# Optimization experiments

Hardware: AMD Instinct MI355X
Metric: run time of the kernel (lower is better)

Reference implementation:

```python
import jax, jax.numpy as jnp
import numpy as np

B, Q, H, W, C = 2, 8192, 64, 64, 64
C9 = C * 9
EPS = 1e-6


def _mlp(x, params):
    # gelu MLP, no activation on last layer (matches repo mlp)
    for Wm, b in params[:-1]:
        x = jax.nn.gelu(x @ Wm + b)
    Wl, bl = params[-1]
    return x @ Wl + bl


def _make_coord(h, w):
    # pixel-center coords in (-1,1); channel 0 = row dim, channel 1 = col dim
    hs = -1.0 + (2.0 * jnp.arange(h, dtype=jnp.float32) + 1.0) / h
    ws = -1.0 + (2.0 * jnp.arange(w, dtype=jnp.float32) + 1.0) / w
    return jnp.stack(jnp.meshgrid(hs, ws, indexing='ij'), axis=0)  # (2,h,w)


def _nearest_gather(feat, coord):
    # F.grid_sample(mode='nearest', align_corners=False) on a (B,1,q,2) grid.
    # feat (B,C,H,W); coord (B,q,2) with [...,0] indexing H, [...,1] indexing W
    h, w = feat.shape[-2], feat.shape[-1]
    ih = jnp.clip(jnp.round((coord[..., 0] + 1.0) * h / 2.0 - 0.5), 0, h - 1).astype(jnp.int32)
    iw = jnp.clip(jnp.round((coord[..., 1] + 1.0) * w / 2.0 - 0.5), 0, w - 1).astype(jnp.int32)
    return jax.vmap(lambda f, a, b: f[:, a, b].T)(feat, ih, iw)  # (B,q,C)


def _unfold3(feat):
    # F.unfold(feat, 3, padding=1).view(B, C*9, H, W): channel-major, kernel row-major
    b, c, h, w = feat.shape
    p = jnp.pad(feat, ((0, 0), (0, 0), (1, 1), (1, 1)))
    patches = jnp.stack([p[:, :, i:i + h, j:j + w] for i in range(3) for j in range(3)], axis=2)
    return patches.reshape(b, c * 9, h, w)


def _forward(inp, coord, scale, enc_w, enc_b, iw0, ib0, iw1, ib1, iw2, ib2,
             sw0, sb0, sw1, sb1, ww0, wb0, ww1, wb1):
    # encoder (stand-in conv3x3, 3 -> C feature channels)
    feat = jax.lax.conv_general_dilated(inp, enc_w, (1, 1), 'SAME',
                                        dimension_numbers=('NCHW', 'OIHW', 'NCHW'))
    feat = feat + enc_b[None, :, None, None]
    feat = _unfold3(feat)  # (B, C*9, H, W)
    bsz, cf, h, w = feat.shape
    fcoord = jnp.broadcast_to(_make_coord(h, w)[None], (bsz, 2, h, w))
    dims = jnp.array([h, w], dtype=feat.dtype)

    tx = (h - 1) / (1.0 - scale[:, 0, 0])  # (B,)
    ty = (w - 1) / (1.0 - scale[:, 0, 1])
    rx, ry = 1.0 / tx, 1.0 / ty
    scale_tok = scale * dims  # (B,q,2)

    imnet_p = [(iw0, ib0), (iw1, ib1), (iw2, ib2)]
    score_p = [(sw0, sb0), (sw1, sb1)]
    weight_p = [(ww0, wb0), (ww1, wb1)]

    preds = []
    for vx in (-1, 1):
        for vy in (-1, 1):
            shift = jnp.stack([vx * rx + EPS, vy * ry + EPS], axis=-1)[:, None, :]  # (B,1,2)
            c = jnp.clip(coord + shift, -1.0 + 1e-6, 1.0 - 1e-6)
            value = _nearest_gather(feat, c)      # (B,q,C*9)
            coord_k = _nearest_gather(fcoord, c)  # (B,q,2)
            rel = (coord - coord_k) * dims        # (B,q,2)
            score = _mlp(rel, score_p)            # (B,q,1) -> broadcast over 3
            mlp_in = jnp.concatenate([rel, scale_tok], axis=-1)  # (B,q,4)
            wmat = _mlp(mlp_in, imnet_p).reshape(bsz, -1, cf, 3)  # (B,q,C*9,3)
            preds.append(jnp.einsum('bqc,bqck->bqk', value, wmat) + score)
    stacked = jnp.stack(preds, axis=-1)  # (B,q,3,4)
    return _mlp(stacked, weight_p)[..., 0]  # (B,q,3)


def setup_inputs() -> dict:
    key = jax.random.key(0)
    ks = jax.random.split(key, 16)
    f32 = jnp.float32

    def wi(k, shape, fan_in):
        return jax.random.normal(k, shape, f32) / np.float32(np.sqrt(fan_in))

    return {
        'inp': jax.random.normal(ks[0], (B, 3, H, W), f32),
        'coord': jax.random.uniform(ks[1], (B, Q, 2), f32, -1.0 + 1e-4, 1.0 - 1e-4),
        'scale': jax.random.uniform(ks[2], (B, Q, 2), f32, 0.01, 0.05),
        'enc_w': wi(ks[3], (C, 3, 3, 3), 27),
        'enc_b': jnp.zeros((C,), f32),
        'iw0': wi(ks[4], (4, 256), 4), 'ib0': jnp.zeros((256,), f32),
        'iw1': wi(ks[5], (256, 256), 256), 'ib1': jnp.zeros((256,), f32),
        'iw2': wi(ks[6], (256, C9 * 3), 256), 'ib2': jnp.zeros((C9 * 3,), f32),
        'sw0': wi(ks[7], (2, 256), 2), 'sb0': jnp.zeros((256,), f32),
        'sw1': wi(ks[8], (256, 1), 256), 'sb1': jnp.zeros((1,), f32),
        'ww0': wi(ks[9], (4, 256), 4), 'wb0': jnp.zeros((256,), f32),
        'ww1': wi(ks[10], (256, 1), 256), 'wb1': jnp.zeros((1,), f32),
    }


def reference(inp, coord, scale, enc_w, enc_b, iw0, ib0, iw1, ib1, iw2, ib2,
              sw0, sb0, sw1, sb1, ww0, wb0, ww1, wb1):
    return _forward(inp, coord, scale, enc_w, enc_b, iw0, ib0, iw1, ib1, iw2, ib2,
                    sw0, sb0, sw1, sb1, ww0, wb0, ww1, wb1)
```

## Files before the change

kernel.cpp:

```cpp
#include <hip/hip_runtime.h>

#define QN 8192
#define CCH 64
#define NROW 65536
#define MR 64
#define NBLK (NROW / MR)
#define H0S 264
#define UW 784
#define SVP 592

typedef _Float16 f16x8 __attribute__((ext_vector_type(8)));
typedef _Float16 f16x4 __attribute__((ext_vector_type(4)));
typedef float f32x4 __attribute__((ext_vector_type(4)));

__device__ __forceinline__ float gelu_f(float x) {
    float x2 = x * x;
    float tt = fmaf(0.044715f, x2, 1.0f);
    float e = __builtin_amdgcn_exp2f(2.3022081597f * x * tt);
    float r = __builtin_amdgcn_rcpf(1.0f + e);
    return x - x * r;
}

__global__ __launch_bounds__(256) void k_pre(const float* __restrict__ inp,
                                             const float* __restrict__ ew,
                                             const float* __restrict__ eb,
                                             const float* __restrict__ coord,
                                             const float* __restrict__ scale,
                                             const float* __restrict__ sw0,
                                             const float* __restrict__ sb0,
                                             const float* __restrict__ sw1,
                                             const float* __restrict__ sb1,
                                             const float* __restrict__ iw1,
                                             const float* __restrict__ iw2,
                                             const float* __restrict__ ib2,
                                             float* __restrict__ featpad,
                                             float4* __restrict__ mlp_in,
                                             int2* __restrict__ ihiw,
                                             float* __restrict__ scoreg,
                                             _Float16* __restrict__ w1tp,
                                             _Float16* __restrict__ w3tp) {
    const int bb = blockIdx.x;
    const int tt0 = threadIdx.x;
    if (bb < 2178) {
        __shared__ float s_ew[1728];
        for (int i = tt0; i < 1728; i += 256) s_ew[i] = ew[i];
        __syncthreads();
        int idx = bb * 256 + tt0;
        const int total = 2 * 66 * 66 * CCH;
        if (idx >= total) return;
        int o = idx & 63; int pix = idx >> 6;
        int xx = pix % 66; int t2 = pix / 66;
        int yy = t2 % 66;  int b = t2 / 66;
        int y = yy - 1, x = xx - 1;
        float acc = 0.0f;
        if (y >= 0 && y < 64 && x >= 0 && x < 64) {
            acc = eb[o];
            for (int i = 0; i < 3; ++i) {
                const float* ip = inp + ((b * 3 + i) * 64) * 64;
                const float* wp = s_ew + (o * 3 + i) * 9;
                #pragma unroll
                for (int ky = 0; ky < 3; ++ky) {
                    int sy = y + ky - 1;
                    if (sy < 0 || sy > 63) continue;
                    #pragma unroll
                    for (int kx = 0; kx < 3; ++kx) {
                        int sx = x + kx - 1;
                        if (sx < 0 || sx > 63) continue;
                        acc += ip[sy * 64 + sx] * wp[ky * 3 + kx];
                    }
                }
            }
        }
        featpad[idx] = acc;
    } else if (bb < 2434) {
        int row = (bb - 2178) * 256 + tt0;
        int v = row & 3;
        int bq = row >> 2;
        int b = bq >> 13;
        float c0 = coord[bq * 2 + 0], c1 = coord[bq * 2 + 1];
        float s0 = scale[bq * 2 + 0], s1 = scale[bq * 2 + 1];
        float s00 = scale[(b * QN) * 2 + 0];
        float s01 = scale[(b * QN) * 2 + 1];
        float rx = (1.0f - s00) / 63.0f;
        float ry = (1.0f - s01) / 63.0f;
        float vx = (v & 2) ? 1.0f : -1.0f;
        float vy = (v & 1) ? 1.0f : -1.0f;
        float cc0 = c0 + vx * rx + 1e-6f;
        float cc1 = c1 + vy * ry + 1e-6f;
        cc0 = fminf(fmaxf(cc0, -1.0f + 1e-6f), 1.0f - 1e-6f);
        cc1 = fminf(fmaxf(cc1, -1.0f + 1e-6f), 1.0f - 1e-6f);
        int ih = (int)rintf((cc0 + 1.0f) * 32.0f - 0.5f);
        int iw = (int)rintf((cc1 + 1.0f) * 32.0f - 0.5f);
        ih = min(max(ih, 0), 63);
        iw = min(max(iw, 0), 63);
        float ck0 = (2.0f * (float)ih + 1.0f) / 64.0f - 1.0f;
        float ck1 = (2.0f * (float)iw + 1.0f) / 64.0f - 1.0f;
        float rel0 = (c0 - ck0) * 64.0f;
        float rel1 = (c1 - ck1) * 64.0f;
        mlp_in[row] = make_float4(rel0, rel1, s0 * 64.0f, s1 * 64.0f);
        ihiw[row] = make_int2(ih, iw);
        float sc = sb1[0];
        #pragma unroll 4
        for (int t2 = 0; t2 < 256; ++t2) {
            float h = gelu_f(fmaf(rel0, sw0[t2], fmaf(rel1, sw0[256 + t2], sb0[t2])));
            sc = fmaf(h, sw1[t2], sc);
        }
        scoreg[row] = sc;
    } else {
        int idx = (bb - 2434) * 256 + tt0;
        if (idx < 451584) {
            int jj = idx & 7, ln = (idx >> 3) & 63;
            int tlkf = idx >> 9;
            int tl = tlkf / 18, kf = tlkf - tl * 18;
            int o = tl * 16 + (ln & 15);
            int v = kf * 32 + (ln >> 4) * 8 + jj;
            int tap = v >> 6, cch = v & 63;
            float val = 0.0f;
            if (o < 768) {
                int j = o & 255, k = o >> 8;
                val = iw2[j * 1728 + (cch * 9 + tap) * 3 + k];
            } else if (o < 771) {
                val = ib2[(cch * 9 + tap) * 3 + (o - 768)];
            }
            w3tp[idx] = (_Float16)val;
        } else {
            int i2 = idx - 451584;
            int j = i2 & 7, ln = (i2 >> 3) & 63, kf = (i2 >> 9) & 7, ct = i2 >> 12;
            int col = ct * 16 + (ln & 15);
            int kk = kf * 32 + (ln >> 4) * 8 + j;
            w1tp[i2] = (_Float16)iw1[kk * 256 + col];
        }
    }
}

__global__ __launch_bounds__(256) void k_u(const float* __restrict__ featpad,
                                           const _Float16* __restrict__ w3tp,
                                           _Float16* __restrict__ u) {
    __shared__ __align__(16) _Float16 s_val[32 * SVP];
    __shared__ int s_dtab[9];
    const int t = threadIdx.x;
    const int wave = t >> 6, lane = t & 63, quad = lane >> 4, l15 = lane & 15;
    if (t < 9) { int dy = t / 3; s_dtab[t] = (dy * 66 + (t - 3 * dy)) * 64; }
    {
        int p = t & 31, half = t >> 5;
        int slot = blockIdx.x * 32 + p;
        int b = slot >> 12, rem = slot & 4095, y = rem >> 6, x = rem & 63;
        int base = ((b * 66 + y) * 66 + x) * 64;
        __syncthreads();
        #pragma unroll
        for (int i = 0; i < 18; ++i) {
            int v0 = half * 72 + i * 4;
            int tap = v0 >> 6, cch = v0 & 63;
            float4 f = *(const float4*)(featpad + base + s_dtab[tap] + cch);
            f16x4 hv = {(_Float16)f.x, (_Float16)f.y, (_Float16)f.z, (_Float16)f.w};
            *(f16x4*)(s_val + p * SVP + v0) = hv;
        }
    }
    __syncthreads();

    const int t0 = (wave == 0) ? 0 : 1 + wave * 12;
    const int nt = (wave == 0) ? 13 : 12;
    #pragma unroll 1
    for (int tt = 0; tt < nt; ++tt) {
        int tl = t0 + tt;
        const _Float16* wp = w3tp + ((size_t)(tl * 18) * 64 + lane) * 8;
        f16x8 bbuf[18];
        #pragma unroll
        for (int kf = 0; kf < 18; ++kf) bbuf[kf] = *(const f16x8*)(wp + (size_t)kf * 512);
        f32x4 ac0 = {0.f, 0.f, 0.f, 0.f}, ac1 = {0.f, 0.f, 0.f, 0.f};
        #pragma unroll
        for (int kf = 0; kf < 18; ++kf) {
            f16x8 a0 = *(const f16x8*)(s_val + l15 * SVP + kf * 32 + quad * 8);
            f16x8 a1 = *(const f16x8*)(s_val + (16 + l15) * SVP + kf * 32 + quad * 8);
            ac0 = __builtin_amdgcn_mfma_f32_16x16x32_f16(a0, bbuf[kf], ac0, 0, 0, 0);
            ac1 = __builtin_amdgcn_mfma_f32_16x16x32_f16(a1, bbuf[kf], ac1, 0, 0, 0);
        }
        size_t pb = (size_t)(blockIdx.x * 32 + quad * 4) * UW + tl * 16 + l15;
        #pragma unroll
        for (int rg = 0; rg < 4; ++rg) u[pb + (size_t)rg * UW] = (_Float16)ac0[rg];
        pb += (size_t)16 * UW;
        #pragma unroll
        for (int rg = 0; rg < 4; ++rg) u[pb + (size_t)rg * UW] = (_Float16)ac1[rg];
    }
}

#define LDX1(B, CT) do { const _Float16* wp_ = w1tp + (size_t)((CT) * 8) * 512 + lane * 8;        \
    _Pragma("unroll") for (int kf_ = 0; kf_ < 4; ++kf_) B[kf_] = *(const f16x8*)(wp_ + kf_ * 512); } while (0)
#define LDY1(B, CT) do { const _Float16* wp_ = w1tp + (size_t)((CT) * 8 + 4) * 512 + lane * 8;    \
    _Pragma("unroll") for (int kf_ = 0; kf_ < 4; ++kf_) B[kf_] = *(const f16x8*)(wp_ + kf_ * 512); } while (0)
#define ZACCB(BV) do { _Pragma("unroll") for (int rt_ = 0; rt_ < 4; ++rt_)                        \
    acc[rt_] = (f32x4){(BV), (BV), (BV), (BV)}; } while (0)
#define MFMAH(B, OFS) do { _Pragma("unroll") for (int kf_ = 0; kf_ < 4; ++kf_)                    \
    { _Pragma("unroll") for (int rt_ = 0; rt_ < 4; ++rt_)                                         \
      acc[rt_] = __builtin_amdgcn_mfma_f32_16x16x32_f16(a[rt_][kf_ + (OFS)], B[kf_], acc[rt_], 0, 0, 0); } } while (0)
#define H1EPI(CT) do { int col_ = (CT) * 16 + l15;                                                \
    _Pragma("unroll") for (int rt_ = 0; rt_ < 4; ++rt_)                                           \
      { _Pragma("unroll") for (int rg_ = 0; rg_ < 4; ++rg_)                                       \
        s_h0[(rt_ * 16 + quad * 4 + rg_) * H0S + col_] = (_Float16)gelu_f(acc[rt_][rg_]); } } while (0)

__global__ __launch_bounds__(256, 2) void k_dot(const float4* __restrict__ mlp_in,
                                                const int2* __restrict__ ihiw,
                                                const float* __restrict__ iw0,
                                                const float* __restrict__ ib0,
                                                const _Float16* __restrict__ w1tp,
                                                const float* __restrict__ ib1,
                                                const _Float16* __restrict__ ubuf,
                                                const float* __restrict__ scoreg,
                                                const float* __restrict__ ww0,
                                                const float* __restrict__ wb0,
                                                const float* __restrict__ ww1,
                                                const float* __restrict__ wb1,
                                                float* __restrict__ out) {
    __shared__ __align__(16) _Float16 s_h0[MR * H0S];
    __shared__ float4 s_min[MR];
    __shared__ int    s_slot[MR];
    __shared__ float  s_pred[MR][3];
    __shared__ float  s_score[MR];
    __shared__ float  s_dred[MR][3][4];
    __shared__ float  s_wred[48][4];

    const int t = threadIdx.x;
    const int wave = t >> 6, lane = t & 63, quad = lane >> 4, l15 = lane & 15;
    const int rowbase = blockIdx.x * MR;

    if (t < MR) {
        int row = rowbase + t;
        s_min[t] = mlp_in[row];
        s_score[t] = scoreg[row];
        int b = row >> 15;
        int2 p = ihiw[row];
        s_slot[t] = (b << 12) + (p.x << 6) + p.y;
    }
    __syncthreads();

    {
        float w0 = iw0[t], w1 = iw0[256 + t], w2 = iw0[512 + t], w3 = iw0[768 + t];
        float bb = ib0[t];
        #pragma unroll 4
        for (int r = 0; r < MR; ++r) {
            float4 m = s_min[r];
            s_h0[r * H0S + t] =
                (_Float16)gelu_f(fmaf(m.x, w0, fmaf(m.y, w1, fmaf(m.z, w2, fmaf(m.w, w3, bb)))));
        }
    }
    __syncthreads();

    const int w4 = wave * 4;
    const float bibA = ib1[(w4 + 0) * 16 + l15];
    const float bibB = ib1[(w4 + 1) * 16 + l15];
    const float bibC = ib1[(w4 + 2) * 16 + l15];
    const float bibD = ib1[(w4 + 3) * 16 + l15];

    f16x8 bX0[4], bX1[4], bY0[4], bY1[4];
    f32x4 acc[4];

    LDX1(bX0, w4);
    LDY1(bY0, w4);
    LDX1(bX1, w4 + 1);

    f16x8 a[4][8];
    #pragma unroll
    for (int rt = 0; rt < 4; ++rt)
        #pragma unroll
        for (int kf = 0; kf < 8; ++kf)
            a[rt][kf] = *(const f16x8*)(s_h0 + (rt * 16 + l15) * H0S + kf * 32 + quad * 8);
    __syncthreads();

    LDY1(bY1, w4 + 1);
    ZACCB(bibA); MFMAH(bX0, 0);
    LDX1(bX0, w4 + 2);
    MFMAH(bY0, 4);
    H1EPI(w4);
    LDY1(bY0, w4 + 2);
    ZACCB(bibB); MFMAH(bX1, 0);
    LDX1(bX1, w4 + 3);
    MFMAH(bY1, 4);
    H1EPI(w4 + 1);
    LDY1(bY1, w4 + 3);
    ZACCB(bibC); MFMAH(bX0, 0);
    MFMAH(bY0, 4);
    H1EPI(w4 + 2);
    ZACCB(bibD); MFMAH(bX1, 0);
    MFMAH(bY1, 4);
    H1EPI(w4 + 3);
    __syncthreads();

    {
        int r = t >> 2, sub = t & 3;
        int j0 = sub * 64;
        size_t sb = (size_t)s_slot[r] * UW;
        float a0 = 0.f, a1 = 0.f, a2 = 0.f;
        #pragma unroll
        for (int g = 0; g < 4; ++g) {
            int j = j0 + g * 16;
            f16x8 hA  = *(const f16x8*)(s_h0 + r * H0S + j);
            f16x8 hB  = *(const f16x8*)(s_h0 + r * H0S + j + 8);
            f16x8 u0A = *(const f16x8*)(ubuf + sb + j);
            f16x8 u0B = *(const f16x8*)(ubuf + sb + j + 8);
            f16x8 u1A = *(const f16x8*)(ubuf + sb + 256 + j);
            f16x8 u1B = *(const f16x8*)(ubuf + sb + 256 + j + 8);
            f16x8 u2A = *(const f16x8*)(ubuf + sb + 512 + j);
            f16x8 u2B = *(const f16x8*)(ubuf + sb + 512 + j + 8);
            #pragma unroll
            for (int e = 0; e < 8; ++e) {
                float hx = (float)hA[e], hy = (float)hB[e];
                a0 = fmaf(hx, (float)u0A[e], a0); a0 = fmaf(hy, (float)u0B[e], a0);
                a1 = fmaf(hx, (float)u1A[e], a1); a1 = fmaf(hy, (float)u1B[e], a1);
                a2 = fmaf(hx, (float)u2A[e], a2); a2 = fmaf(hy, (float)u2B[e], a2);
            }
        }
        s_dred[r][0][sub] = a0;
        s_dred[r][1][sub] = a1;
        s_dred[r][2][sub] = a2;
    }
    __syncthreads();
    if (t < 192) {
        int r = t / 3, k = t - 3 * r;
        float s = s_dred[r][k][0] + s_dred[r][k][1] + s_dred[r][k][2] + s_dred[r][k][3]
                + (float)ubuf[(size_t)s_slot[r] * UW + 768 + k];
        s_pred[r][k] = s;
    }
    __syncthreads();

    if (t < 192) {
        int o = t >> 2, sub = t & 3;
        int bql = o / 3, k = o - 3 * bql;
        float x0 = s_pred[bql * 4 + 0][k] + s_score[bql * 4 + 0];
        float x1 = s_pred[bql * 4 + 1][k] + s_score[bql * 4 + 1];
        float x2 = s_pred[bql * 4 + 2][k] + s_score[bql * 4 + 2];
        float x3 = s_pred[bql * 4 + 3][k] + s_score[bql * 4 + 3];
        float acc2 = 0.0f;
        int j0 = sub * 64;
        #pragma unroll 4
        for (int j = j0; j < j0 + 64; ++j) {
            float h = gelu_f(fmaf(x0, ww0[j], fmaf(x1, ww0[256 + j],
                          fmaf(x2, ww0[512 + j], fmaf(x3, ww0[768 + j], wb0[j])))));
            acc2 = fmaf(h, ww1[j], acc2);
        }
        s_wred[o][sub] = acc2;
    }
    __syncthreads();
    if (t < 48) {
        int bql = t / 3, k = t - 3 * bql;
        float r2 = s_wred[t][0] + s_wred[t][1] + s_wred[t][2] + s_wred[t][3] + wb1[0];
        out[(blockIdx.x * 16 + bql) * 3 + k] = r2;
    }
}

extern "C" void kernel_launch(void* const* d_in, const int* in_sizes, int n_in,
                              void* d_out, int out_size, void* d_ws, size_t ws_size,
                              hipStream_t stream) {
    const float* inp   = (const float*)d_in[0];
    const float* coord = (const float*)d_in[1];
    const float* scale = (const float*)d_in[2];
    const float* ew    = (const float*)d_in[3];
    const float* eb    = (const float*)d_in[4];
    const float* iw0   = (const float*)d_in[5];
    const float* ib0   = (const float*)d_in[6];
    const float* iw1   = (const float*)d_in[7];
    const float* ib1   = (const float*)d_in[8];
    const float* iw2   = (const float*)d_in[9];
    const float* ib2   = (const float*)d_in[10];
    const float* sw0   = (const float*)d_in[11];
    const float* sb0   = (const float*)d_in[12];
    const float* sw1   = (const float*)d_in[13];
    const float* sb1   = (const float*)d_in[14];
    const float* ww0   = (const float*)d_in[15];
    const float* wb0   = (const float*)d_in[16];
    const float* ww1   = (const float*)d_in[17];
    const float* wb1   = (const float*)d_in[18];
    float* out = (float*)d_out;

    char* ws = (char*)d_ws;
    float*     featpad = (float*)(ws + 0);
    float4*    mlp_in  = (float4*)(ws + 2230272);
    int2*      ihiw    = (int2*)(ws + 3278848);
    float*     scoreg  = (float*)(ws + 3803136);
    _Float16*  w1tp    = (_Float16*)(ws + 4065280);
    _Float16*  w3tp    = (_Float16*)(ws + 4196352);
    _Float16*  u       = (_Float16*)(ws + 5099520);

    k_pre<<<dim3(4454), dim3(256), 0, stream>>>(inp, ew, eb, coord, scale,
                                                sw0, sb0, sw1, sb1, iw1, iw2, ib2,
                                                featpad, mlp_in, ihiw, scoreg,
                                                w1tp, w3tp);
    k_u<<<dim3(256), dim3(256), 0, stream>>>(featpad, w3tp, u);
    k_dot<<<dim3(NBLK), dim3(256), 0, stream>>>(mlp_in, ihiw, iw0, ib0, w1tp, ib1,
                                                u, scoreg, ww0, wb0, ww1, wb1, out);
}
```

Baseline: 224.5 us.

## Halve rows per block in k_dot and use fdot2 for gathered dot products

Rows per block in the fused MLP/dot kernel drop from 64 to 32. This halves the per-wave MFMA A-fragment registers and the shared-memory tile, so launch bounds can ask for 4 blocks per CU instead of 2, and twice as many blocks are launched. The gathered dot stage now uses 8 threads per row and packed f16 dot2 instructions instead of converting each element and issuing scalar FMAs. In exchange, each block reloads the w1 B-fragments for half as many rows, and fdot2 accumulation may round slightly differently.

```diff
diff --git a/kernel.cpp b/kernel.cpp
--- a/kernel.cpp
+++ b/kernel.cpp
@@ -3,7 +3,7 @@
 #define QN 8192
 #define CCH 64
 #define NROW 65536
-#define MR 64
+#define MR 32
 #define NBLK (NROW / MR)
 #define H0S 264
 #define UW 784
@@ -11,7 +11,20 @@
 
 typedef _Float16 f16x8 __attribute__((ext_vector_type(8)));
 typedef _Float16 f16x4 __attribute__((ext_vector_type(4)));
+typedef _Float16 f16x2 __attribute__((ext_vector_type(2)));
 typedef float f32x4 __attribute__((ext_vector_type(4)));
+
+#if __has_builtin(__builtin_amdgcn_fdot2)
+#define FDOT2(A, B, C) __builtin_amdgcn_fdot2((A), (B), (C), false)
+#else
+#define FDOT2(A, B, C) fmaf((float)(A)[1], (float)(B)[1], fmaf((float)(A)[0], (float)(B)[0], (C)))
+#endif
+#define DOT8(H, U, ACC) do {                                                                      \
+    ACC = FDOT2(((f16x2){(H)[0], (H)[1]}), ((f16x2){(U)[0], (U)[1]}), ACC);                       \
+    ACC = FDOT2(((f16x2){(H)[2], (H)[3]}), ((f16x2){(U)[2], (U)[3]}), ACC);                       \
+    ACC = FDOT2(((f16x2){(H)[4], (H)[5]}), ((f16x2){(U)[4], (U)[5]}), ACC);                       \
+    ACC = FDOT2(((f16x2){(H)[6], (H)[7]}), ((f16x2){(U)[6], (U)[7]}), ACC);                       \
+} while (0)
 
 __device__ __forceinline__ float gelu_f(float x) {
     float x2 = x * x;
@@ -188,17 +201,17 @@
     _Pragma("unroll") for (int kf_ = 0; kf_ < 4; ++kf_) B[kf_] = *(const f16x8*)(wp_ + kf_ * 512); } while (0)
 #define LDY1(B, CT) do { const _Float16* wp_ = w1tp + (size_t)((CT) * 8 + 4) * 512 + lane * 8;    \
     _Pragma("unroll") for (int kf_ = 0; kf_ < 4; ++kf_) B[kf_] = *(const f16x8*)(wp_ + kf_ * 512); } while (0)
-#define ZACCB(BV) do { _Pragma("unroll") for (int rt_ = 0; rt_ < 4; ++rt_)                        \
+#define ZACCB(BV) do { _Pragma("unroll") for (int rt_ = 0; rt_ < 2; ++rt_)                        \
     acc[rt_] = (f32x4){(BV), (BV), (BV), (BV)}; } while (0)
 #define MFMAH(B, OFS) do { _Pragma("unroll") for (int kf_ = 0; kf_ < 4; ++kf_)                    \
-    { _Pragma("unroll") for (int rt_ = 0; rt_ < 4; ++rt_)                                         \
+    { _Pragma("unroll") for (int rt_ = 0; rt_ < 2; ++rt_)                                         \
       acc[rt_] = __builtin_amdgcn_mfma_f32_16x16x32_f16(a[rt_][kf_ + (OFS)], B[kf_], acc[rt_], 0, 0, 0); } } while (0)
 #define H1EPI(CT) do { int col_ = (CT) * 16 + l15;                                                \
-    _Pragma("unroll") for (int rt_ = 0; rt_ < 4; ++rt_)                                           \
+    _Pragma("unroll") for (int rt_ = 0; rt_ < 2; ++rt_)                                           \
       { _Pragma("unroll") for (int rg_ = 0; rg_ < 4; ++rg_)                                       \
         s_h0[(rt_ * 16 + quad * 4 + rg_) * H0S + col_] = (_Float16)gelu_f(acc[rt_][rg_]); } } while (0)
 
-__global__ __launch_bounds__(256, 2) void k_dot(const float4* __restrict__ mlp_in,
+__global__ __launch_bounds__(256, 4) void k_dot(const float4* __restrict__ mlp_in,
                                                 const int2* __restrict__ ihiw,
                                                 const float* __restrict__ iw0,
                                                 const float* __restrict__ ib0,
@@ -216,8 +229,8 @@
     __shared__ int    s_slot[MR];
     __shared__ float  s_pred[MR][3];
     __shared__ float  s_score[MR];
-    __shared__ float  s_dred[MR][3][4];
-    __shared__ float  s_wred[48][4];
+    __shared__ float  s_dred[MR][3][8];
+    __shared__ float  s_wred[24][4];
 
     const int t = threadIdx.x;
     const int wave = t >> 6, lane = t & 63, quad = lane >> 4, l15 = lane & 15;
@@ -252,15 +265,15 @@
     const float bibD = ib1[(w4 + 3) * 16 + l15];
 
     f16x8 bX0[4], bX1[4], bY0[4], bY1[4];
-    f32x4 acc[4];
+    f32x4 acc[2];
 
     LDX1(bX0, w4);
     LDY1(bY0, w4);
     LDX1(bX1, w4 + 1);
 
-    f16x8 a[4][8];
+    f16x8 a[2][8];
     #pragma unroll
-    for (int rt = 0; rt < 4; ++rt)
+    for (int rt = 0; rt < 2; ++rt)
         #pragma unroll
         for (int kf = 0; kf < 8; ++kf)
             a[rt][kf] = *(const f16x8*)(s_h0 + (rt * 16 + l15) * H0S + kf * 32 + quad * 8);
@@ -286,43 +299,36 @@
     __syncthreads();
 
     {
-        int r = t >> 2, sub = t & 3;
-        int j0 = sub * 64;
-        size_t sb = (size_t)s_slot[r] * UW;
+        int r = t >> 3, sub = t & 7;
+        int j0 = sub * 32;
+        const _Float16* hb = s_h0 + r * H0S + j0;
+        const _Float16* ub = ubuf + (size_t)s_slot[r] * UW + j0;
         float a0 = 0.f, a1 = 0.f, a2 = 0.f;
         #pragma unroll
-        for (int g = 0; g < 4; ++g) {
-            int j = j0 + g * 16;
-            f16x8 hA  = *(const f16x8*)(s_h0 + r * H0S + j);
-            f16x8 hB  = *(const f16x8*)(s_h0 + r * H0S + j + 8);
-            f16x8 u0A = *(const f16x8*)(ubuf + sb + j);
-            f16x8 u0B = *(const f16x8*)(ubuf + sb + j + 8);
-            f16x8 u1A = *(const f16x8*)(ubuf + sb + 256 + j);
-            f16x8 u1B = *(const f16x8*)(ubuf + sb + 256 + j + 8);
-            f16x8 u2A = *(const f16x8*)(ubuf + sb + 512 + j);
-            f16x8 u2B = *(const f16x8*)(ubuf + sb + 512 + j + 8);
-            #pragma unroll
-            for (int e = 0; e < 8; ++e) {
-                float hx = (float)hA[e], hy = (float)hB[e];
-                a0 = fmaf(hx, (float)u0A[e], a0); a0 = fmaf(hy, (float)u0B[e], a0);
-                a1 = fmaf(hx, (float)u1A[e], a1); a1 = fmaf(hy, (float)u1B[e], a1);
-                a2 = fmaf(hx, (float)u2A[e], a2); a2 = fmaf(hy, (float)u2B[e], a2);
-            }
+        for (int c = 0; c < 4; ++c) {
+            f16x8 h8 = *(const f16x8*)(hb + c * 8);
+            f16x8 u0 = *(const f16x8*)(ub + c * 8);
+            f16x8 u1 = *(const f16x8*)(ub + 256 + c * 8);
+            f16x8 u2 = *(const f16x8*)(ub + 512 + c * 8);
+            DOT8(h8, u0, a0);
+            DOT8(h8, u1, a1);
+            DOT8(h8, u2, a2);
         }
         s_dred[r][0][sub] = a0;
         s_dred[r][1][sub] = a1;
         s_dred[r][2][sub] = a2;
     }
     __syncthreads();
-    if (t < 192) {
+    if (t < 96) {
         int r = t / 3, k = t - 3 * r;
-        float s = s_dred[r][k][0] + s_dred[r][k][1] + s_dred[r][k][2] + s_dred[r][k][3]
-                + (float)ubuf[(size_t)s_slot[r] * UW + 768 + k];
+        float s = (float)ubuf[(size_t)s_slot[r] * UW + 768 + k];
+        #pragma unroll
+        for (int q = 0; q < 8; ++q) s += s_dred[r][k][q];
         s_pred[r][k] = s;
     }
     __syncthreads();
 
-    if (t < 192) {
+    if (t < 96) {
         int o = t >> 2, sub = t & 3;
         int bql = o / 3, k = o - 3 * bql;
         float x0 = s_pred[bql * 4 + 0][k] + s_score[bql * 4 + 0];
@@ -340,10 +346,10 @@
         s_wred[o][sub] = acc2;
     }
     __syncthreads();
-    if (t < 48) {
+    if (t < 24) {
         int bql = t / 3, k = t - 3 * bql;
         float r2 = s_wred[t][0] + s_wred[t][1] + s_wred[t][2] + s_wred[t][3] + wb1[0];
-        out[(blockIdx.x * 16 + bql) * 3 + k] = r2;
+        out[(blockIdx.x * 8 + bql) * 3 + k] = r2;
     }
 }
 
```

Result: slower. 231.9 us (+3.3%).
